# Optimization experiments

Hardware: AMD Instinct MI355X
Metric: run time of the kernel (lower is better)

Reference implementation:

```python
import jax, jax.numpy as jnp
from jax import lax
import numpy as np
import math

B, H, W = 4, 64, 64
D_MODEL, D_STATE, D_CONV, EXPAND, K = 96, 16, 3, 2, 4
D_INNER = EXPAND * D_MODEL          # 192
DT_RANK = math.ceil(D_MODEL / 16)   # 6


def setup_inputs() -> dict:
    key = jax.random.key(0)
    ks = jax.random.split(key, 12)
    s = 0.02
    rgb = jax.random.normal(ks[0], (B, H, W, D_MODEL), jnp.float32)
    t = jax.random.normal(ks[1], (B, H, W, D_MODEL), jnp.float32)
    in_proj1_w = jax.random.normal(ks[2], (2 * D_INNER, D_MODEL), jnp.float32) * s
    in_proj2_w = jax.random.normal(ks[3], (2 * D_INNER, D_MODEL), jnp.float32) * s
    conv1_w = jax.random.normal(ks[4], (D_INNER, 1, D_CONV, D_CONV), jnp.float32) * s
    conv1_b = jnp.zeros((D_INNER,), jnp.float32)
    conv2_w = jax.random.normal(ks[5], (D_INNER, 1, D_CONV, D_CONV), jnp.float32) * s
    conv2_b = jnp.zeros((D_INNER,), jnp.float32)
    x_proj_weight = jax.random.normal(ks[6], (K, DT_RANK + 2 * D_STATE, D_INNER), jnp.float32) * s
    lim = DT_RANK ** -0.5
    dt_projs_weight = jax.random.uniform(ks[7], (K, D_INNER, DT_RANK), jnp.float32, -lim, lim)
    dt = jnp.exp(jax.random.uniform(ks[8], (K, D_INNER), jnp.float32)
                 * (math.log(0.1) - math.log(0.001)) + math.log(0.001))
    dt = jnp.clip(dt, 1e-4, None)
    dt_projs_bias = dt + jnp.log(-jnp.expm1(-dt))  # inverse softplus
    A_logs = jnp.tile(jnp.log(jnp.arange(1, D_STATE + 1, dtype=jnp.float32))[None], (K * D_INNER, 1))
    Ds = jnp.ones((K * D_INNER,), jnp.float32)
    norm1_w = jnp.ones((D_INNER,), jnp.float32); norm1_b = jnp.zeros((D_INNER,), jnp.float32)
    norm2_w = jnp.ones((D_INNER,), jnp.float32); norm2_b = jnp.zeros((D_INNER,), jnp.float32)
    out_proj1_w = jax.random.normal(ks[9], (D_MODEL, D_INNER), jnp.float32) * s
    out_proj2_w = jax.random.normal(ks[10], (D_MODEL, D_INNER), jnp.float32) * s
    return dict(rgb=rgb, t=t, in_proj1_w=in_proj1_w, in_proj2_w=in_proj2_w,
                conv1_w=conv1_w, conv1_b=conv1_b, conv2_w=conv2_w, conv2_b=conv2_b,
                x_proj_weight=x_proj_weight, dt_projs_weight=dt_projs_weight,
                dt_projs_bias=dt_projs_bias, A_logs=A_logs, Ds=Ds,
                norm1_w=norm1_w, norm1_b=norm1_b, norm2_w=norm2_w, norm2_b=norm2_b,
                out_proj1_w=out_proj1_w, out_proj2_w=out_proj2_w)


def _dwconv(x, w, b):
    # x: (B, C, H, W), depthwise 3x3, padding=1
    y = lax.conv_general_dilated(x, w, (1, 1), 'SAME',
                                 feature_group_count=x.shape[1],
                                 dimension_numbers=('NCHW', 'OIHW', 'NCHW'))
    return y + b[None, :, None, None]


def _ln(x, w, b, eps=1e-5):
    m = x.mean(-1, keepdims=True)
    v = ((x - m) ** 2).mean(-1, keepdims=True)
    return (x - m) / jnp.sqrt(v + eps) * w + b


def _cross_scan(x):
    # x: (B, C, H, W) -> (B, 4, C, L): row-major, col-major, and their reverses
    Bz, C, Hh, Ww = x.shape
    L = Hh * Ww
    xr = x.reshape(Bz, C, L)
    xt = x.transpose(0, 1, 3, 2).reshape(Bz, C, L)
    xh = jnp.stack([xr, xt], 1)                        # (B,2,C,L)
    return jnp.concatenate([xh, jnp.flip(xh, -1)], 1)  # (B,4,C,L)


def _cross_merge(y, Hh, Ww):
    # y: (B, 4, C, L) -> (B, C, L); undo scan directions then sum
    Bz, _, C, L = y.shape
    inv = jnp.flip(y[:, 2:4], -1)                      # (B,2,C,L)
    wh = y[:, 1].reshape(Bz, C, Ww, Hh).transpose(0, 1, 3, 2).reshape(Bz, C, L)
    invwh = inv[:, 1].reshape(Bz, C, Ww, Hh).transpose(0, 1, 3, 2).reshape(Bz, C, L)
    return y[:, 0] + inv[:, 0] + wh + invwh


def _selective_scan(u, delta, A, Bs, Cs, Ds, delta_bias):
    # u, delta: (B, K, C, L2); A: (K, C, N); Bs, Cs: (B, K, N, L2); Ds: (K, C)
    Bz, Kk, C, L2 = u.shape
    N = A.shape[-1]
    delta = jax.nn.softplus(delta + delta_bias[None, :, :, None])

    def step(h, inp):
        d_l, u_l, B_l, C_l = inp               # (B,K,C),(B,K,C),(B,K,N),(B,K,N)
        dA = jnp.exp(d_l[..., None] * A[None])            # (B,K,C,N)
        dBu = (d_l * u_l)[..., None] * B_l[:, :, None, :]  # (B,K,C,N)
        h = h * dA + dBu
        y = jnp.einsum('bkcn,bkn->bkc', h, C_l)
        return h, y

    h0 = jnp.zeros((Bz, Kk, C, N), u.dtype)
    seq = (delta.transpose(3, 0, 1, 2), u.transpose(3, 0, 1, 2),
           Bs.transpose(3, 0, 1, 2), Cs.transpose(3, 0, 1, 2))
    _, ys = lax.scan(step, h0, seq)            # (L2, B, K, C)
    y = ys.transpose(1, 2, 3, 0)               # (B, K, C, L2)
    return y + u * Ds[None, :, :, None]


def _forward_core(x1, x2, x_proj_weight, dt_projs_weight, dt_projs_bias, A_logs, Ds):
    # x1, x2: (B, C, H, W)
    Bz, C, Hh, Ww = x1.shape
    L = Hh * Ww
    rgb4 = _cross_scan(x1)                     # (B,4,C,L)
    t4 = _cross_scan(x2)
    # interleave modalities along sequence: [..., rgb_i, t_i, ...] length 2L
    xs = jnp.stack([rgb4, t4], -1).reshape(Bz, K, C, 2 * L)
    x_dbl = jnp.einsum('bkdl,kcd->bkcl', xs, x_proj_weight)
    dts, Bm, Cm = jnp.split(x_dbl, [DT_RANK, DT_RANK + D_STATE], axis=2)
    dts = jnp.einsum('bkrl,kdr->bkdl', dts, dt_projs_weight)   # (B,K,C,2L)
    As = -jnp.exp(A_logs.astype(jnp.float32)).reshape(K, C, D_STATE)
    y = _selective_scan(xs, dts, As, Bm, Cm, Ds.reshape(K, C), dt_projs_bias)
    y = y.reshape(Bz, K, C, L, 2)
    y_rgb = _cross_merge(y[..., 0], Hh, Ww)    # (B,C,L)
    y_t = _cross_merge(y[..., 1], Hh, Ww)
    return y_rgb, y_t


def reference(rgb, t, in_proj1_w, in_proj2_w, conv1_w, conv1_b, conv2_w, conv2_b,
              x_proj_weight, dt_projs_weight, dt_projs_bias, A_logs, Ds,
              norm1_w, norm1_b, norm2_w, norm2_b, out_proj1_w, out_proj2_w):
    Bz, Hh, Ww, _ = rgb.shape
    x1, z1 = jnp.split(rgb @ in_proj1_w.T, 2, -1)
    x2, z2 = jnp.split(t @ in_proj2_w.T, 2, -1)
    x1 = jax.nn.silu(_dwconv(x1.transpose(0, 3, 1, 2), conv1_w, conv1_b))
    x2 = jax.nn.silu(_dwconv(x2.transpose(0, 3, 1, 2), conv2_w, conv2_b))
    y_rgb, y_t = _forward_core(x1, x2, x_proj_weight, dt_projs_weight,
                               dt_projs_bias, A_logs, Ds)
    y_rgb = _ln(y_rgb.transpose(0, 2, 1).reshape(Bz, Hh, Ww, D_INNER), norm1_w, norm1_b)
    y_t = _ln(y_t.transpose(0, 2, 1).reshape(Bz, Hh, Ww, D_INNER), norm2_w, norm2_b)
    out1 = (y_rgb * jax.nn.silu(z1)) @ out_proj1_w.T
    out2 = (y_t * jax.nn.silu(z2)) @ out_proj2_w.T
    return out1, out2
```

## Files before the change

### kernel.cpp

```cpp
#include <hip/hip_runtime.h>
#include <math.h>

#define BB   4
#define LL   4096
#define L2T  8192
#define DM   96
#define CI   192
#define KD   4
#define NN   16
#define RR   6
#define BKT  16
#define SS   64
#define TT   128
#define DBLS 40

#define OFF_XPRE1 0
#define OFF_XPRE2 3145728
#define OFF_Z1    6291456
#define OFF_Z2    9437184
#define OFF_X1C   12582912
#define OFF_X2C   15728640
#define OFF_DBL   18874368
#define OFF_MERG  24117248
#define OFF_DSUM  30408704

__global__ __launch_bounds__(256)
void k_inproj(const float* __restrict__ rgb, const float* __restrict__ tin,
              const float* __restrict__ w1, const float* __restrict__ w2,
              float* __restrict__ xp1, float* __restrict__ xp2,
              float* __restrict__ zz1, float* __restrict__ zz2) {
  int mb = blockIdx.x;
  int nb = blockIdx.y;
  int m  = blockIdx.z;
  const float* in = m ? tin : rgb;
  const float* w  = (m ? w2 : w1) + nb * 96 * DM;
  __shared__ float As[64][100];
  __shared__ float Ws[96][98];
  int t = threadIdx.x;
  const float4* asrc = (const float4*)(in + (size_t)mb * 64 * DM);
  for (int i = t; i < 1536; i += 256) {
    int r = i / 24, kk = (i % 24) * 4;
    *(float4*)&As[r][kk] = asrc[i];
  }
  const float2* wsrc = (const float2*)w;
  for (int i = t; i < 4608; i += 256) {
    int r = i / 48, kk = (i % 48) * 2;
    *(float2*)&Ws[r][kk] = wsrc[i];
  }
  __syncthreads();
  int tc = t & 15, tr = t >> 4;
  float acc[4][6] = {};
  for (int k = 0; k < 96; k += 2) {
    float2 a[4], b[6];
#pragma unroll
    for (int i = 0; i < 4; i++) a[i] = *(const float2*)&As[tr * 4 + i][k];
#pragma unroll
    for (int j = 0; j < 6; j++) b[j] = *(const float2*)&Ws[tc * 6 + j][k];
#pragma unroll
    for (int i = 0; i < 4; i++)
#pragma unroll
      for (int j = 0; j < 6; j++) {
        acc[i][j] = fmaf(a[i].x, b[j].x, acc[i][j]);
        acc[i][j] = fmaf(a[i].y, b[j].y, acc[i][j]);
      }
  }
  float* dst = (nb < 2) ? (m ? xp2 : xp1) : (m ? zz2 : zz1);
  int colbase = (nb & 1) * 96 + tc * 6;
#pragma unroll
  for (int i = 0; i < 4; i++) {
    size_t bl = (size_t)mb * 64 + tr * 4 + i;
#pragma unroll
    for (int j = 0; j < 6; j++)
      dst[bl * CI + colbase + j] = acc[i][j];
  }
}

__global__ __launch_bounds__(256)
void k_conv(const float* __restrict__ xp1, const float* __restrict__ xp2,
            const float* __restrict__ c1w, const float* __restrict__ c1b,
            const float* __restrict__ c2w, const float* __restrict__ c2b,
            float* __restrict__ o1, float* __restrict__ o2) {
  int m = blockIdx.y;
  const float* in = m ? xp2 : xp1;
  const float* cw = m ? c2w : c1w;
  const float* cb = m ? c2b : c1b;
  float* out = m ? o2 : o1;
  int idx = blockIdx.x * 256 + threadIdx.x;
  int c = idx % CI;
  int bl = idx / CI;
  int b = bl / LL, l = bl % LL;
  int hh = l >> 6, ww = l & 63;
  float a = cb[c];
#pragma unroll
  for (int di = 0; di < 3; di++) {
    int h2 = hh + di - 1;
    if ((unsigned)h2 >= 64u) continue;
#pragma unroll
    for (int dj = 0; dj < 3; dj++) {
      int w2 = ww + dj - 1;
      if ((unsigned)w2 >= 64u) continue;
      a = fmaf(in[(b * LL + h2 * 64 + w2) * CI + c], cw[c * 9 + di * 3 + dj], a);
    }
  }
  out[idx] = a / (1.f + __expf(-a));
}

__global__ __launch_bounds__(256)
void k_dbl(const float* __restrict__ x1c, const float* __restrict__ x2c,
           const float* __restrict__ wx, float* __restrict__ dbl) {
  int pt = blockIdx.x;
  int bk = blockIdx.y;
  int b = bk >> 2, k = bk & 3;
  __shared__ float As[64][100];
  __shared__ float Ws[40][100];
  int t = threadIdx.x;
  int tc = t & 7, tr = t >> 3;
  float acc[2][5] = {};
  for (int kc = 0; kc < 2; kc++) {
    if (kc) __syncthreads();
    for (int i = t; i < 1536; i += 256) {
      int r = i / 24, kk = (i % 24) * 4;
      int l2 = pt * 64 + r;
      int mm = l2 & 1, l = l2 >> 1;
      int lt = (k >= 2) ? (LL - 1 - l) : l;
      int sp = (k & 1) ? (((lt & 63) << 6) | (lt >> 6)) : lt;
      const float* src = (mm ? x2c : x1c) + ((size_t)(b * LL + sp)) * CI + kc * 96;
      *(float4*)&As[r][kk] = *(const float4*)(src + kk);
    }
    for (int i = t; i < 960; i += 256) {
      int r = i / 24, kk = (i % 24) * 4;
      float4 v;
      if (r < 38) v = *(const float4*)&wx[(size_t)(k * 38 + r) * CI + kc * 96 + kk];
      else        v = float4{0.f, 0.f, 0.f, 0.f};
      *(float4*)&Ws[r][kk] = v;
    }
    __syncthreads();
    for (int kk2 = 0; kk2 < 96; kk2 += 2) {
      float2 a[2], bv[5];
#pragma unroll
      for (int i = 0; i < 2; i++) a[i] = *(const float2*)&As[tr * 2 + i][kk2];
#pragma unroll
      for (int j = 0; j < 5; j++) bv[j] = *(const float2*)&Ws[tc * 5 + j][kk2];
#pragma unroll
      for (int i = 0; i < 2; i++)
#pragma unroll
        for (int j = 0; j < 5; j++) {
          acc[i][j] = fmaf(a[i].x, bv[j].x, acc[i][j]);
          acc[i][j] = fmaf(a[i].y, bv[j].y, acc[i][j]);
        }
    }
  }
#pragma unroll
  for (int i = 0; i < 2; i++) {
    size_t row = (size_t)bk * L2T + pt * 64 + tr * 2 + i;
#pragma unroll
    for (int j = 0; j < 5; j++) {
      int cc = tc * 5 + j;
      if (cc < 38) dbl[row * DBLS + cc] = acc[i][j];
    }
  }
}

template<int PASS>
__global__ __launch_bounds__(64)
void k_scan(const float* __restrict__ x1c, const float* __restrict__ x2c,
            const float* __restrict__ dbl,
            const float* __restrict__ dtw, const float* __restrict__ dtb,
            const float* __restrict__ alogs, const float* __restrict__ dsv,
            float* __restrict__ hend, float* __restrict__ dsum,
            const float* __restrict__ hin, float* __restrict__ merged) {
  int bid = blockIdx.x;
  int s  = bid & 63;
  int bk = (bid >> 6) & 15;
  int cg = bid >> 10;
  int b = bk >> 2, kdir = bk & 3;
  int lane = threadIdx.x;
  int c = cg * 64 + lane;
  int kc = kdir * CI + c;

  float w2r0 = dtw[kc * RR + 0], w2r1 = dtw[kc * RR + 1], w2r2 = dtw[kc * RR + 2];
  float w2r3 = dtw[kc * RR + 3], w2r4 = dtw[kc * RR + 4], w2r5 = dtw[kc * RR + 5];
  float bias = dtb[kc];
  float Dv   = (PASS == 2) ? dsv[kc] : 0.f;
  float Areg[NN];
#pragma unroll
  for (int n = 0; n < NN; n++) Areg[n] = -__expf(alogs[kc * NN + n]);
  float A1 = Areg[0];
  int ok = 1;
#pragma unroll
  for (int n = 1; n < NN; n++) {
    float want = A1 * (float)(n + 1);
    if (!(fabsf(Areg[n] - want) <= fabsf(want) * 1e-3f + 1e-6f)) ok = 0;
  }
  const bool structured = (__all(ok) != 0);

  float h[NN];
  if (PASS == 2) {
    int base = ((s * BKT + bk) * CI + c) * NN;
#pragma unroll
    for (int n = 0; n < NN; n++) h[n] = hin[base + n];
  } else {
#pragma unroll
    for (int n = 0; n < NN; n++) h[n] = 0.f;
  }
  float dacc = 0.f;

  const float* dp = dbl + (size_t)(bk * L2T + s * TT) * DBLS;
  const float* u1b = x1c + (size_t)b * LL * CI + c;
  const float* u2b = x2c + (size_t)b * LL * CI + c;

  auto spmap = [&](int l) -> int {
    int lt = (kdir >= 2) ? (LL - 1 - l) : l;
    return (kdir & 1) ? (((lt & 63) << 6) | (lt >> 6)) : lt;
  };

  auto step = [&](const float* dr, float u, float& y) {
    float x = bias;
    x = fmaf(dr[0], w2r0, x); x = fmaf(dr[1], w2r1, x); x = fmaf(dr[2], w2r2, x);
    x = fmaf(dr[3], w2r3, x); x = fmaf(dr[4], w2r4, x); x = fmaf(dr[5], w2r5, x);
    float delta = (x > 15.f) ? x : __logf(1.f + __expf(x));
    float du = delta * u;
    float y0 = 0.f, y1 = 0.f, y2 = 0.f, y3 = 0.f;
    if (structured) {
      float r  = __expf(delta * A1);
      float r2 = r * r, r3 = r2 * r, r4 = r2 * r2;
      float r6 = r4 * r2, r8 = r4 * r4;
      float pw[NN];
      pw[0] = r;       pw[1] = r2;      pw[2] = r3;      pw[3] = r4;
      pw[4] = r4 * r;  pw[5] = r6;      pw[6] = r4 * r3; pw[7] = r8;
      pw[8] = r8 * r;  pw[9] = r8 * r2; pw[10] = r8 * r3; pw[11] = r8 * r4;
      pw[12] = r8 * pw[4]; pw[13] = r8 * r6; pw[14] = r8 * pw[6]; pw[15] = r8 * r8;
#pragma unroll
      for (int n = 0; n < NN; n++) {
        h[n] = fmaf(h[n], pw[n], du * dr[6 + n]);
        if (PASS == 2) {
          float* yp = (n & 2) ? ((n & 1) ? &y3 : &y2) : ((n & 1) ? &y1 : &y0);
          *yp = fmaf(h[n], dr[22 + n], *yp);
        }
      }
    } else {
#pragma unroll
      for (int n = 0; n < NN; n++) {
        float dA = __expf(delta * Areg[n]);
        h[n] = fmaf(h[n], dA, du * dr[6 + n]);
        if (PASS == 2) {
          float* yp = (n & 2) ? ((n & 1) ? &y3 : &y2) : ((n & 1) ? &y1 : &y0);
          *yp = fmaf(h[n], dr[22 + n], *yp);
        }
      }
    }
    if (PASS == 1) dacc += delta;
    else y = fmaf(u, Dv, (y0 + y1) + (y2 + y3));
  };

  int l0 = (s * TT) >> 1;
  int sp = spmap(l0);
  float u1 = u1b[(size_t)sp * CI];
  float u2 = u2b[(size_t)sp * CI];
#pragma unroll 2
  for (int p = 0; p < TT / 2; p++) {
    int spn = 0; float u1n = 0.f, u2n = 0.f;
    if (p + 1 < TT / 2) {
      spn = spmap(l0 + p + 1);
      u1n = u1b[(size_t)spn * CI];
      u2n = u2b[(size_t)spn * CI];
    }
    const float* dr = dp + (size_t)(2 * p) * DBLS;
    float ya, yb;
    step(dr, u1, ya);
    step(dr + DBLS, u2, yb);
    if (PASS == 2) {
      float* mrow = merged + (size_t)(b * LL + sp) * (2 * CI) + c;
      atomicAdd(mrow, ya);
      atomicAdd(mrow + CI, yb);
    }
    sp = spn; u1 = u1n; u2 = u2n;
  }

  if (PASS == 1) {
    int base = ((s * BKT + bk) * CI + c) * NN;
#pragma unroll
    for (int n = 0; n < NN; n++) hend[base + n] = h[n];
    dsum[(s * BKT + bk) * CI + c] = dacc;
  }
}

__global__ __launch_bounds__(256)
void k_prop(const float* __restrict__ hend, const float* __restrict__ dsum,
            const float* __restrict__ alogs, float* __restrict__ hin) {
  int idx = blockIdx.x * 256 + threadIdx.x;
  int n = idx & 15;
  int rest = idx >> 4;
  int c = rest % CI;
  int bk = rest / CI;
  int k = bk & 3;
  float A = -__expf(alogs[(k * CI + c) * NN + n]);
  float h = 0.f;
  for (int s = 0; s < SS; s++) {
    int cell = (s * BKT + bk) * CI + c;
    hin[cell * NN + n] = h;
    float ap = __expf(A * dsum[cell]);
    h = h * ap + hend[cell * NN + n];
  }
}

__global__ __launch_bounds__(192)
void k_lngate(float* __restrict__ merged,
              const float* __restrict__ z1, const float* __restrict__ z2,
              const float* __restrict__ n1w, const float* __restrict__ n1b,
              const float* __restrict__ n2w, const float* __restrict__ n2b) {
  int bid = blockIdx.x;
  int m = bid & 1;
  int bl = bid >> 1;
  int c = threadIdx.x;
  float v = merged[(size_t)bid * CI + c];
  float s1 = v, s2 = v * v;
  for (int o = 32; o > 0; o >>= 1) {
    s1 += __shfl_xor(s1, o);
    s2 += __shfl_xor(s2, o);
  }
  __shared__ float red[2][3];
  int wv = threadIdx.x >> 6, ln = threadIdx.x & 63;
  if (ln == 0) { red[0][wv] = s1; red[1][wv] = s2; }
  __syncthreads();
  float S1 = red[0][0] + red[0][1] + red[0][2];
  float S2 = red[1][0] + red[1][1] + red[1][2];
  float mean = S1 * (1.f / CI);
  float var = S2 * (1.f / CI) - mean * mean;
  float rstd = rsqrtf(var + 1e-5f);
  const float* nw = m ? n2w : n1w;
  const float* nb = m ? n2b : n1b;
  float vn = (v - mean) * rstd * nw[c] + nb[c];
  float z = (m ? z2 : z1)[(size_t)bl * CI + c];
  float g = vn * (z / (1.f + __expf(-z)));
  merged[(size_t)bid * CI + c] = g;
}

__global__ __launch_bounds__(256)
void k_outproj(const float* __restrict__ g,
               const float* __restrict__ w1, const float* __restrict__ w2,
               float* __restrict__ out) {
  int mb = blockIdx.x;
  int m  = blockIdx.y;
  const float* w = m ? w2 : w1;
  __shared__ float As[64][100];
  __shared__ float Ws[96][98];
  int t = threadIdx.x;
  int tc = t & 15, tr = t >> 4;
  float acc[4][6] = {};
  for (int kc = 0; kc < 2; kc++) {
    if (kc) __syncthreads();
    for (int i = t; i < 1536; i += 256) {
      int r = i / 24, kk = (i % 24) * 4;
      *(float4*)&As[r][kk] =
          *(const float4*)&g[((size_t)(mb * 64 + r) * 2 + m) * CI + kc * 96 + kk];
    }
    for (int i = t; i < 4608; i += 256) {
      int r = i / 48, kk = (i % 48) * 2;
      *(float2*)&Ws[r][kk] = *(const float2*)&w[(size_t)r * CI + kc * 96 + kk];
    }
    __syncthreads();
    for (int k = 0; k < 96; k += 2) {
      float2 a[4], b[6];
#pragma unroll
      for (int i = 0; i < 4; i++) a[i] = *(const float2*)&As[tr * 4 + i][k];
#pragma unroll
      for (int j = 0; j < 6; j++) b[j] = *(const float2*)&Ws[tc * 6 + j][k];
#pragma unroll
      for (int i = 0; i < 4; i++)
#pragma unroll
        for (int j = 0; j < 6; j++) {
          acc[i][j] = fmaf(a[i].x, b[j].x, acc[i][j]);
          acc[i][j] = fmaf(a[i].y, b[j].y, acc[i][j]);
        }
    }
  }
  float* outp = out + (size_t)m * (BB * LL * DM);
#pragma unroll
  for (int i = 0; i < 4; i++) {
    size_t bl = (size_t)mb * 64 + tr * 4 + i;
#pragma unroll
    for (int j = 0; j < 6; j++)
      outp[bl * DM + tc * 6 + j] = acc[i][j];
  }
}

extern "C" void kernel_launch(void* const* d_in, const int* in_sizes, int n_in,
                              void* d_out, int out_size, void* d_ws, size_t ws_size,
                              hipStream_t stream) {
  const float* rgb = (const float*)d_in[0];
  const float* tin = (const float*)d_in[1];
  const float* ip1 = (const float*)d_in[2];
  const float* ip2 = (const float*)d_in[3];
  const float* c1w = (const float*)d_in[4];
  const float* c1b = (const float*)d_in[5];
  const float* c2w = (const float*)d_in[6];
  const float* c2b = (const float*)d_in[7];
  const float* wx  = (const float*)d_in[8];
  const float* dtw = (const float*)d_in[9];
  const float* dtb = (const float*)d_in[10];
  const float* alg = (const float*)d_in[11];
  const float* Dsp = (const float*)d_in[12];
  const float* n1w = (const float*)d_in[13];
  const float* n1b = (const float*)d_in[14];
  const float* n2w = (const float*)d_in[15];
  const float* n2b = (const float*)d_in[16];
  const float* op1 = (const float*)d_in[17];
  const float* op2 = (const float*)d_in[18];

  float* ws = (float*)d_ws;
  float* xp1 = ws + OFF_XPRE1;
  float* xp2 = ws + OFF_XPRE2;
  float* z1  = ws + OFF_Z1;
  float* z2  = ws + OFF_Z2;
  float* x1c = ws + OFF_X1C;
  float* x2c = ws + OFF_X2C;
  float* dbl = ws + OFF_DBL;
  float* mg  = ws + OFF_MERG;
  float* dsm = ws + OFF_DSUM;
  float* he  = ws + OFF_XPRE1;
  float* hi  = ws + OFF_XPRE2;
  float* out = (float*)d_out;

  hipMemsetAsync(mg, 0, (size_t)6291456 * sizeof(float), stream);

  k_inproj<<<dim3(256, 4, 2), 256, 0, stream>>>(rgb, tin, ip1, ip2, xp1, xp2, z1, z2);
  k_conv<<<dim3(12288, 2), 256, 0, stream>>>(xp1, xp2, c1w, c1b, c2w, c2b, x1c, x2c);
  k_dbl<<<dim3(128, 16), 256, 0, stream>>>(x1c, x2c, wx, dbl);
  k_scan<1><<<SS * BKT * 3, 64, 0, stream>>>(x1c, x2c, dbl, dtw, dtb, alg, Dsp, he, dsm, hi, mg);
  k_prop<<<192, 256, 0, stream>>>(he, dsm, alg, hi);
  k_scan<2><<<SS * BKT * 3, 64, 0, stream>>>(x1c, x2c, dbl, dtw, dtb, alg, Dsp, he, dsm, hi, mg);
  k_lngate<<<BB * LL * 2, 192, 0, stream>>>(mg, z1, z2, n1w, n1b, n2w, n2b);
  k_outproj<<<dim3(256, 2), 256, 0, stream>>>(mg, op1, op2, out);
}
```

Measured before the change: 470.9 us.

## Split scan state dimension across two blocks to double scan parallelism

```diff
diff --git a/kernel.cpp b/kernel.cpp
--- a/kernel.cpp
+++ b/kernel.cpp
@@ -8,6 +8,7 @@
 #define CI   192
 #define KD   4
 #define NN   16
+#define NH   8
 #define RR   6
 #define BKT  16
 #define SS   64
@@ -172,36 +173,42 @@
   int bid = blockIdx.x;
   int s  = bid & 63;
   int bk = (bid >> 6) & 15;
-  int cg = bid >> 10;
+  int rest = bid >> 10;
+  int cg = rest % 3;
+  int half = rest / 3;
   int b = bk >> 2, kdir = bk & 3;
   int lane = threadIdx.x;
   int c = cg * 64 + lane;
   int kc = kdir * CI + c;
+  int nb0 = half * NH;
 
   float w2r0 = dtw[kc * RR + 0], w2r1 = dtw[kc * RR + 1], w2r2 = dtw[kc * RR + 2];
   float w2r3 = dtw[kc * RR + 3], w2r4 = dtw[kc * RR + 4], w2r5 = dtw[kc * RR + 5];
   float bias = dtb[kc];
-  float Dv   = (PASS == 2) ? dsv[kc] : 0.f;
-  float Areg[NN];
-#pragma unroll
-  for (int n = 0; n < NN; n++) Areg[n] = -__expf(alogs[kc * NN + n]);
-  float A1 = Areg[0];
+  float Dv   = (PASS == 2 && half == 0) ? dsv[kc] : 0.f;
+  float a16[NN];
+#pragma unroll
+  for (int n = 0; n < NN; n++) a16[n] = -__expf(alogs[kc * NN + n]);
+  float A1 = a16[0];
   int ok = 1;
 #pragma unroll
   for (int n = 1; n < NN; n++) {
     float want = A1 * (float)(n + 1);
-    if (!(fabsf(Areg[n] - want) <= fabsf(want) * 1e-3f + 1e-6f)) ok = 0;
+    if (!(fabsf(a16[n] - want) <= fabsf(want) * 1e-3f + 1e-6f)) ok = 0;
   }
   const bool structured = (__all(ok) != 0);
-
-  float h[NN];
+  float Areg[NH];
+#pragma unroll
+  for (int j = 0; j < NH; j++) Areg[j] = a16[nb0 + j];
+
+  float h[NH];
   if (PASS == 2) {
-    int base = ((s * BKT + bk) * CI + c) * NN;
-#pragma unroll
-    for (int n = 0; n < NN; n++) h[n] = hin[base + n];
+    int base = ((s * BKT + bk) * CI + c) * NN + nb0;
+#pragma unroll
+    for (int j = 0; j < NH; j++) h[j] = hin[base + j];
   } else {
 #pragma unroll
-    for (int n = 0; n < NN; n++) h[n] = 0.f;
+    for (int j = 0; j < NH; j++) h[j] = 0.f;
   }
   float dacc = 0.f;
 
@@ -220,37 +227,36 @@
     x = fmaf(dr[3], w2r3, x); x = fmaf(dr[4], w2r4, x); x = fmaf(dr[5], w2r5, x);
     float delta = (x > 15.f) ? x : __logf(1.f + __expf(x));
     float du = delta * u;
-    float y0 = 0.f, y1 = 0.f, y2 = 0.f, y3 = 0.f;
+    float y0 = 0.f, y1 = 0.f;
     if (structured) {
       float r  = __expf(delta * A1);
       float r2 = r * r, r3 = r2 * r, r4 = r2 * r2;
-      float r6 = r4 * r2, r8 = r4 * r4;
-      float pw[NN];
-      pw[0] = r;       pw[1] = r2;      pw[2] = r3;      pw[3] = r4;
-      pw[4] = r4 * r;  pw[5] = r6;      pw[6] = r4 * r3; pw[7] = r8;
-      pw[8] = r8 * r;  pw[9] = r8 * r2; pw[10] = r8 * r3; pw[11] = r8 * r4;
-      pw[12] = r8 * pw[4]; pw[13] = r8 * r6; pw[14] = r8 * pw[6]; pw[15] = r8 * r8;
-#pragma unroll
-      for (int n = 0; n < NN; n++) {
-        h[n] = fmaf(h[n], pw[n], du * dr[6 + n]);
+      float r5 = r4 * r, r6 = r4 * r2, r7 = r4 * r3, r8 = r4 * r4;
+      float basep = half ? r8 : 1.f;
+      float pw[NH];
+      pw[0] = basep * r;  pw[1] = basep * r2; pw[2] = basep * r3; pw[3] = basep * r4;
+      pw[4] = basep * r5; pw[5] = basep * r6; pw[6] = basep * r7; pw[7] = basep * r8;
+#pragma unroll
+      for (int j = 0; j < NH; j++) {
+        h[j] = fmaf(h[j], pw[j], du * dr[6 + nb0 + j]);
         if (PASS == 2) {
-          float* yp = (n & 2) ? ((n & 1) ? &y3 : &y2) : ((n & 1) ? &y1 : &y0);
-          *yp = fmaf(h[n], dr[22 + n], *yp);
+          if (j & 1) y1 = fmaf(h[j], dr[22 + nb0 + j], y1);
+          else       y0 = fmaf(h[j], dr[22 + nb0 + j], y0);
         }
       }
     } else {
 #pragma unroll
-      for (int n = 0; n < NN; n++) {
-        float dA = __expf(delta * Areg[n]);
-        h[n] = fmaf(h[n], dA, du * dr[6 + n]);
+      for (int j = 0; j < NH; j++) {
+        float dA = __expf(delta * Areg[j]);
+        h[j] = fmaf(h[j], dA, du * dr[6 + nb0 + j]);
         if (PASS == 2) {
-          float* yp = (n & 2) ? ((n & 1) ? &y3 : &y2) : ((n & 1) ? &y1 : &y0);
-          *yp = fmaf(h[n], dr[22 + n], *yp);
+          if (j & 1) y1 = fmaf(h[j], dr[22 + nb0 + j], y1);
+          else       y0 = fmaf(h[j], dr[22 + nb0 + j], y0);
         }
       }
     }
     if (PASS == 1) dacc += delta;
-    else y = fmaf(u, Dv, (y0 + y1) + (y2 + y3));
+    else y = fmaf(u, Dv, y0 + y1);
   };
 
   int l0 = (s * TT) >> 1;
@@ -278,10 +284,10 @@
   }
 
   if (PASS == 1) {
-    int base = ((s * BKT + bk) * CI + c) * NN;
-#pragma unroll
-    for (int n = 0; n < NN; n++) hend[base + n] = h[n];
-    dsum[(s * BKT + bk) * CI + c] = dacc;
+    int base = ((s * BKT + bk) * CI + c) * NN + nb0;
+#pragma unroll
+    for (int j = 0; j < NH; j++) hend[base + j] = h[j];
+    if (half == 0) dsum[(s * BKT + bk) * CI + c] = dacc;
   }
 }
 
@@ -427,9 +433,9 @@
   k_inproj<<<dim3(256, 4, 2), 256, 0, stream>>>(rgb, tin, ip1, ip2, xp1, xp2, z1, z2);
   k_conv<<<dim3(12288, 2), 256, 0, stream>>>(xp1, xp2, c1w, c1b, c2w, c2b, x1c, x2c);
   k_dbl<<<dim3(128, 16), 256, 0, stream>>>(x1c, x2c, wx, dbl);
-  k_scan<1><<<SS * BKT * 3, 64, 0, stream>>>(x1c, x2c, dbl, dtw, dtb, alg, Dsp, he, dsm, hi, mg);
+  k_scan<1><<<SS * BKT * 3 * 2, 64, 0, stream>>>(x1c, x2c, dbl, dtw, dtb, alg, Dsp, he, dsm, hi, mg);
   k_prop<<<192, 256, 0, stream>>>(he, dsm, alg, hi);
-  k_scan<2><<<SS * BKT * 3, 64, 0, stream>>>(x1c, x2c, dbl, dtw, dtb, alg, Dsp, he, dsm, hi, mg);
+  k_scan<2><<<SS * BKT * 3 * 2, 64, 0, stream>>>(x1c, x2c, dbl, dtw, dtb, alg, Dsp, he, dsm, hi, mg);
   k_lngate<<<BB * LL * 2, 192, 0, stream>>>(mg, z1, z2, n1w, n1b, n2w, n2b);
   k_outproj<<<dim3(256, 2), 256, 0, stream>>>(mg, op1, op2, out);
 }
```

Measured after the change: 543.6 us. 1.15x slower.
